# Optimization experiments

Measured on AMD Instinct MI355X. Metric: run time of the kernel, lower is better.

Reference implementation:

```python
import jax, jax.numpy as jnp
import numpy as np

B, D_IN, H1, H2, D_OUT = 1024, 2048, 4096, 4096, 1024

def setup_inputs() -> dict:
    key = jax.random.key(0)
    ks = jax.random.split(key, 8)
    scale = lambda fan_in: 1.0 / np.sqrt(fan_in)
    x  = jax.random.normal(ks[0], (B, D_IN), dtype=jnp.float32)
    W1 = jax.random.normal(ks[1], (H1, D_IN), dtype=jnp.float32) * scale(D_IN)
    b1 = jax.random.normal(ks[2], (H1,), dtype=jnp.float32) * scale(D_IN)
    W2 = jax.random.normal(ks[3], (H2, H1), dtype=jnp.float32) * scale(H1)
    b2 = jax.random.normal(ks[4], (H2,), dtype=jnp.float32) * scale(H1)
    W3 = jax.random.normal(ks[5], (D_OUT, H2), dtype=jnp.float32) * scale(H2)
    b3 = jax.random.normal(ks[6], (D_OUT,), dtype=jnp.float32) * scale(H2)
    b_taus = jnp.array([2.0, 1.0, 0.5], dtype=jnp.float32)
    return {"x": x, "W1": W1, "b1": b1, "W2": W2, "b2": b2, "W3": W3, "b3": b3, "b_taus": b_taus, "T": 10}

def reference(x, W1, b1, W2, b2, W3, b3, b_taus, T):
    # x: [B, D_IN] (already flat). betas are scalar sigmoid gates, constant over time.
    beta1, beta2, beta3 = jax.nn.sigmoid(b_taus)
    s1 = jnp.zeros((x.shape[0], W1.shape[0]), dtype=x.dtype)
    s2 = jnp.zeros((x.shape[0], W2.shape[0]), dtype=x.dtype)
    s3 = jnp.zeros((x.shape[0], W3.shape[0]), dtype=x.dtype)

    def step(carry, _):
        s1, s2, s3 = carry
        d1 = jax.nn.relu(x @ W1.T + b1)
        s1 = beta1 * s1 + (1 - beta1) * d1
        d2 = jax.nn.relu(s1 @ W2.T + b2)
        s2 = beta2 * s2 + (1 - beta2) * d2
        d3 = s2 @ W3.T + b3
        s3 = beta3 * s3 + (1 - beta3) * d3
        return (s1, s2, s3), None

    (s1, s2, s3), _ = jax.lax.scan(step, (s1, s2, s3), None, length=T)
    return s3
```

## Files before the change

kernel.cpp:

```cpp
#include <hip/hip_runtime.h>
#include <hip/hip_bf16.h>
#include <stdint.h>

#define AS_GLOBAL __attribute__((address_space(1)))
#define AS_LDS    __attribute__((address_space(3)))

typedef __attribute__((ext_vector_type(8))) short  bf16x8;
typedef __attribute__((ext_vector_type(4))) float  f32x4;
typedef __attribute__((ext_vector_type(4))) short  s16x4;
typedef __attribute__((ext_vector_type(8))) short  s16x8;

__device__ __forceinline__ void gload_lds16(const void* g, void* l) {
    __builtin_amdgcn_global_load_lds((AS_GLOBAL const void*)g, (AS_LDS void*)l, 16, 0, 0);
}

__device__ __forceinline__ void cast_pair(const float* __restrict__ s,
                                          __hip_bfloat16* __restrict__ d, long p) {
    f32x4 a = ((const f32x4*)s)[p * 2];
    f32x4 b = ((const f32x4*)s)[p * 2 + 1];
    union { s16x8 p8; __hip_bfloat16 h[8]; } u;
    u.h[0] = __float2bfloat16(a.x); u.h[1] = __float2bfloat16(a.y);
    u.h[2] = __float2bfloat16(a.z); u.h[3] = __float2bfloat16(a.w);
    u.h[4] = __float2bfloat16(b.x); u.h[5] = __float2bfloat16(b.y);
    u.h[6] = __float2bfloat16(b.z); u.h[7] = __float2bfloat16(b.w);
    ((s16x8*)d)[p] = u.p8;
}

__global__ void cast_a_k(const float* __restrict__ x,  __hip_bfloat16* __restrict__ xb,
                         const float* __restrict__ W1, __hip_bfloat16* __restrict__ W1b) {
    const long nx = 262144, ntot = 1310720, stride = 1280 * 256;
    long t = (long)blockIdx.x * 256 + threadIdx.x;
    for (long p = t; p < ntot; p += stride) {
        if (p < nx) cast_pair(x, xb, p);
        else        cast_pair(W1, W1b, p - nx);
    }
}

template <int FUSECAST>
__global__ __launch_bounds__(256, 3)
void gemm_btk(const __hip_bfloat16* __restrict__ A,
              const __hip_bfloat16* __restrict__ Bm,
              __hip_bfloat16* __restrict__ P,
              const int M, const int N, const int kchunk, const int S,
              const float* __restrict__ cs1, __hip_bfloat16* __restrict__ cd1, const long cn1,
              const float* __restrict__ cs2, __hip_bfloat16* __restrict__ cd2, const long cn2)
{
    __shared__ __hip_bfloat16 As[128 * 64];
    __shared__ __hip_bfloat16 Bs[128 * 64];

    const int tid = threadIdx.x;
    const int bn = blockIdx.x, bm = blockIdx.y, z = blockIdx.z;

    if (FUSECAST && z < FUSECAST) {
        const long nb     = (long)gridDim.x * gridDim.y;
        const long stride = FUSECAST * nb * 256;
        long t = ((long)z * nb + (long)bm * gridDim.x + bn) * 256 + tid;
        const long ntot = cn1 + cn2;
        for (long p = t; p < ntot; p += stride) {
            if (p < cn1) cast_pair(cs1, cd1, p);
            else         cast_pair(cs2, cd2, p - cn1);
        }
        return;
    }
    const int kz = z - FUSECAST;

    const int lane = tid & 63;
    const int wave = tid >> 6;
    const int wm   = wave >> 1, wn = wave & 1;
    const int lm   = lane & 15, lq = lane >> 4;

    const int K  = kchunk * S;
    const int k0 = kz * kchunk;

    const int rlo  = lane >> 3;
    const int gsw8 = (((lane & 7) ^ rlo) << 3);

    const __hip_bfloat16* Ag = A  + (size_t)(bm * 128) * K;
    const __hip_bfloat16* Bg = Bm + (size_t)(bn * 128) * K;

    f32x4 acc[4][4];
    #pragma unroll
    for (int i = 0; i < 4; ++i)
        #pragma unroll
        for (int j = 0; j < 4; ++j)
            acc[i][j] = (f32x4){0.f, 0.f, 0.f, 0.f};

    for (int kt = k0; kt < k0 + kchunk; kt += 64) {
        __syncthreads();
        #pragma unroll
        for (int c = 0; c < 4; ++c) {
            const int chunk = wave * 4 + c;
            const int row   = chunk * 8 + rlo;
            gload_lds16(Ag + (size_t)row * K + kt + gsw8, As + chunk * 512);
            gload_lds16(Bg + (size_t)row * K + kt + gsw8, Bs + chunk * 512);
        }
        __syncthreads();
        #pragma unroll
        for (int kk = 0; kk < 2; ++kk) {
            const int sl = (((kk * 4 + lq) ^ (lm & 7)) << 3);
            bf16x8 af[4], bf[4];
            #pragma unroll
            for (int i = 0; i < 4; ++i)
                af[i] = *(const bf16x8*)(As + (wm * 64 + i * 16 + lm) * 64 + sl);
            #pragma unroll
            for (int j = 0; j < 4; ++j)
                bf[j] = *(const bf16x8*)(Bs + (wn * 64 + j * 16 + lm) * 64 + sl);
            #pragma unroll
            for (int i = 0; i < 4; ++i)
                #pragma unroll
                for (int j = 0; j < 4; ++j)
                    acc[i][j] = __builtin_amdgcn_mfma_f32_16x16x32_bf16(af[i], bf[j], acc[i][j], 0, 0, 0);
        }
    }

    __hip_bfloat16* Pz = P + (size_t)kz * M * N;
    const int row0 = bm * 128 + wm * 64;
    const int colb = bn * 128 + wn * 64 + lm;
    #pragma unroll
    for (int j = 0; j < 4; ++j) {
        const int col = colb + j * 16;
        #pragma unroll
        for (int i = 0; i < 4; ++i)
            #pragma unroll
            for (int r = 0; r < 4; ++r) {
                const int row = row0 + i * 16 + lq * 4 + r;
                Pz[(size_t)row * N + col] = __float2bfloat16(acc[i][j][r]);
            }
    }
}

template <int TT>
__device__ __forceinline__ void tcollapse_coef(float be1, float be2, float be3,
                                               float* __restrict__ c, float* __restrict__ w) {
    float g[TT + 1];
    g[TT] = 1.f;
    float p3 = 1.f;
    #pragma unroll
    for (int u = TT - 1; u >= 1; --u) {
        p3 *= be3;
        g[u] = be2 * g[u + 1] + p3;
    }
    const float s = (1.f - be2) * (1.f - be3);
    float p1 = 1.f;
    #pragma unroll
    for (int u = 1; u <= TT; ++u) {
        p1 *= be1;
        c[u - 1] = 1.f - p1;
        w[u - 1] = s * g[u];
    }
}

template <int MODE>
__global__ void reduce_k(const __hip_bfloat16* __restrict__ P, const int S,
                         void* __restrict__ outv, const long MN, const int N,
                         const float* __restrict__ bias,
                         const float* __restrict__ b_taus,
                         const int* __restrict__ Tp)
{
    long i8 = (long)blockIdx.x * 256 + threadIdx.x;
    long i  = i8 * 8;
    float a[8] = {0.f, 0.f, 0.f, 0.f, 0.f, 0.f, 0.f, 0.f};
    for (int s = 0; s < S; ++s) {
        union { s16x8 p8; __hip_bfloat16 h[8]; } u;
        u.p8 = *(const s16x8*)(P + (size_t)s * MN + i);
        #pragma unroll
        for (int c = 0; c < 8; ++c) a[c] += __bfloat162float(u.h[c]);
    }
    const int col = (int)(i % N);
    float bb[8];
    #pragma unroll
    for (int c = 0; c < 8; ++c) bb[c] = bias[col + c];

    if constexpr (MODE == 0) {
        union { s16x8 p8; __hip_bfloat16 h[8]; } u;
        #pragma unroll
        for (int c = 0; c < 8; ++c)
            u.h[c] = __float2bfloat16(fmaxf(a[c] + bb[c], 0.f));
        ((s16x8*)outv)[i8] = u.p8;
    } else if constexpr (MODE == 1) {
        const int   T   = *Tp;
        const float be1 = 1.f / (1.f + expf(-b_taus[0]));
        const float be2 = 1.f / (1.f + expf(-b_taus[1]));
        const float be3 = 1.f / (1.f + expf(-b_taus[2]));
        union { s16x8 p8; __hip_bfloat16 h[8]; } u;
        if (T == 10) {
            float c10[10], w10[10];
            tcollapse_coef<10>(be1, be2, be3, c10, w10);
            #pragma unroll
            for (int c = 0; c < 8; ++c) {
                float za = 0.f;
                #pragma unroll
                for (int t = 0; t < 10; ++t)
                    za += w10[t] * fmaxf(fmaf(c10[t], a[c], bb[c]), 0.f);
                u.h[c] = __float2bfloat16(za);
            }
        } else {
            #pragma unroll
            for (int c = 0; c < 8; ++c) {
                float p1 = 1.f, s2 = 0.f, za = 0.f;
                for (int t = 0; t < T; ++t) {
                    p1 *= be1;
                    const float d2 = fmaxf(fmaf(1.f - p1, a[c], bb[c]), 0.f);
                    s2 = be2 * s2 + (1.f - be2) * d2;
                    za = be3 * za + (1.f - be3) * s2;
                }
                u.h[c] = __float2bfloat16(za);
            }
        }
        ((s16x8*)outv)[i8] = u.p8;
    } else {
        const int   T   = *Tp;
        const float be3 = 1.f / (1.f + expf(-b_taus[2]));
        float g = 0.f;
        for (int t = 0; t < T; ++t) g = be3 * g + (1.f - be3);
        f32x4 o0, o1;
        o0.x = a[0] + g * bb[0]; o0.y = a[1] + g * bb[1];
        o0.z = a[2] + g * bb[2]; o0.w = a[3] + g * bb[3];
        o1.x = a[4] + g * bb[4]; o1.y = a[5] + g * bb[5];
        o1.z = a[6] + g * bb[6]; o1.w = a[7] + g * bb[7];
        ((f32x4*)outv)[i8 * 2]     = o0;
        ((f32x4*)outv)[i8 * 2 + 1] = o1;
    }
}

extern "C" void kernel_launch(void* const* d_in, const int* in_sizes, int n_in,
                              void* d_out, int out_size, void* d_ws, size_t ws_size,
                              hipStream_t stream) {
    const float* x      = (const float*)d_in[0];
    const float* W1     = (const float*)d_in[1];
    const float* b1     = (const float*)d_in[2];
    const float* W2     = (const float*)d_in[3];
    const float* b2     = (const float*)d_in[4];
    const float* W3     = (const float*)d_in[5];
    const float* b3     = (const float*)d_in[6];
    const float* b_taus = (const float*)d_in[7];
    const int*   Tp     = (const int*)d_in[8];

    const int B = 1024, DIN = 2048, H1 = 4096, H2 = 4096, DOUT = 1024;
    const long MB = 1024 * 1024;

    char* ws = (char*)d_ws;
    __hip_bfloat16* xb  = (__hip_bfloat16*)(ws + 0);
    __hip_bfloat16* W1b = (__hip_bfloat16*)(ws + 4 * MB);
    __hip_bfloat16* W2b = (__hip_bfloat16*)(ws + 20 * MB);
    __hip_bfloat16* W3b = (__hip_bfloat16*)(ws + 52 * MB);
    __hip_bfloat16* D1b = (__hip_bfloat16*)(ws + 60 * MB);
    __hip_bfloat16* Sb  = (__hip_bfloat16*)(ws + 68 * MB);
    __hip_bfloat16* P1  = (__hip_bfloat16*)(ws + 76 * MB);
    __hip_bfloat16* P2  = (__hip_bfloat16*)(ws + 92 * MB);
    __hip_bfloat16* P3  = (__hip_bfloat16*)(ws + 124 * MB);

    cast_a_k<<<dim3(1280), dim3(256), 0, stream>>>(x, xb, W1, W1b);

    gemm_btk<1><<<dim3(H1 / 128, B / 128, 1 + 2), 256, 0, stream>>>(
        xb, W1b, P1, B, H1, DIN / 2, 2,
        W2, W2b, (long)H2 * H1 / 8, W3, W3b, (long)DOUT * H2 / 8);
    reduce_k<0><<<dim3(2048), 256, 0, stream>>>(P1, 2, (void*)D1b, (long)B * H1, H1, b1, nullptr, nullptr);

    gemm_btk<0><<<dim3(H2 / 128, B / 128, 4), 256, 0, stream>>>(
        D1b, W2b, P2, B, H2, H1 / 4, 4, nullptr, nullptr, 0, nullptr, nullptr, 0);
    reduce_k<1><<<dim3(2048), 256, 0, stream>>>(P2, 4, (void*)Sb, (long)B * H2, H2, b2, b_taus, Tp);

    gemm_btk<0><<<dim3(DOUT / 128, B / 128, 8), 256, 0, stream>>>(
        Sb, W3b, P3, B, DOUT, H2 / 8, 8, nullptr, nullptr, 0, nullptr, nullptr, 0);
    reduce_k<2><<<dim3(512), 256, 0, stream>>>(P3, 8, d_out, (long)B * DOUT, DOUT, b3, b_taus, Tp);
}
```

Before: 250.6 us.

## Double-buffer LDS in GEMM, remap blocks per XCD, halve layer-2 split-K

The GEMM kernel now keeps two LDS buffers for each operand. It issues the global-to-LDS loads for the next K tile before computing on the current one, which halves the barriers per tile and overlaps loads with MFMA work. Thread blocks are remapped so that consecutive hardware block IDs, which round-robin across the 8 XCDs, land on contiguous column tiles within each XCD, aiming for better L2 reuse. The second GEMM drops from 4 to 2 split-K slices, which shrinks the partial-sum buffer and the reduce work, and occupancy bounds are lowered from 3 to 2 blocks to fit the doubled LDS use.

After: 254.1 us. Within noise of the previous version (+1.4%).

```diff
diff --git a/kernel.cpp b/kernel.cpp
--- a/kernel.cpp
+++ b/kernel.cpp
@@ -37,7 +37,7 @@
 }
 
 template <int FUSECAST>
-__global__ __launch_bounds__(256, 3)
+__global__ __launch_bounds__(256, 2)
 void gemm_btk(const __hip_bfloat16* __restrict__ A,
               const __hip_bfloat16* __restrict__ Bm,
               __hip_bfloat16* __restrict__ P,
@@ -45,11 +45,12 @@
               const float* __restrict__ cs1, __hip_bfloat16* __restrict__ cd1, const long cn1,
               const float* __restrict__ cs2, __hip_bfloat16* __restrict__ cd2, const long cn2)
 {
-    __shared__ __hip_bfloat16 As[128 * 64];
-    __shared__ __hip_bfloat16 Bs[128 * 64];
+    __shared__ __hip_bfloat16 As[2][128 * 64];
+    __shared__ __hip_bfloat16 Bs[2][128 * 64];
 
     const int tid = threadIdx.x;
-    const int bn = blockIdx.x, bm = blockIdx.y, z = blockIdx.z;
+    int bn = blockIdx.x, bm = blockIdx.y;
+    const int z = blockIdx.z;
 
     if (FUSECAST && z < FUSECAST) {
         const long nb     = (long)gridDim.x * gridDim.y;
@@ -64,6 +65,16 @@
     }
     const int kz = z - FUSECAST;
 
+    const int Gx = gridDim.x;
+    if ((Gx & 7) == 0) {
+        const int bnx = Gx >> 3;
+        const int lid = bm * Gx + bn;
+        const int xcd = lid & 7;
+        const int ix  = lid >> 3;
+        bn = xcd * bnx + (ix % bnx);
+        bm = ix / bnx;
+    }
+
     const int lane = tid & 63;
     const int wave = tid >> 6;
     const int wm   = wave >> 1, wn = wave & 1;
@@ -78,38 +89,55 @@
     const __hip_bfloat16* Ag = A  + (size_t)(bm * 128) * K;
     const __hip_bfloat16* Bg = Bm + (size_t)(bn * 128) * K;
 
-    f32x4 acc[4][4];
-    #pragma unroll
-    for (int i = 0; i < 4; ++i)
-        #pragma unroll
-        for (int j = 0; j < 4; ++j)
-            acc[i][j] = (f32x4){0.f, 0.f, 0.f, 0.f};
-
-    for (int kt = k0; kt < k0 + kchunk; kt += 64) {
-        __syncthreads();
+    auto stage = [&](int d, int kt) {
         #pragma unroll
         for (int c = 0; c < 4; ++c) {
             const int chunk = wave * 4 + c;
             const int row   = chunk * 8 + rlo;
-            gload_lds16(Ag + (size_t)row * K + kt + gsw8, As + chunk * 512);
-            gload_lds16(Bg + (size_t)row * K + kt + gsw8, Bs + chunk * 512);
-        }
-        __syncthreads();
+            gload_lds16(Ag + (size_t)row * K + kt + gsw8, &As[d][chunk * 512]);
+            gload_lds16(Bg + (size_t)row * K + kt + gsw8, &Bs[d][chunk * 512]);
+        }
+    };
+
+    stage(0, k0);
+
+    f32x4 acc[4][4];
+    #pragma unroll
+    for (int i = 0; i < 4; ++i)
+        #pragma unroll
+        for (int j = 0; j < 4; ++j)
+            acc[i][j] = (f32x4){0.f, 0.f, 0.f, 0.f};
+
+    auto compute = [&](int d) {
         #pragma unroll
         for (int kk = 0; kk < 2; ++kk) {
             const int sl = (((kk * 4 + lq) ^ (lm & 7)) << 3);
-            bf16x8 af[4], bf[4];
+            bf16x8 af[4], bq[4];
             #pragma unroll
             for (int i = 0; i < 4; ++i)
-                af[i] = *(const bf16x8*)(As + (wm * 64 + i * 16 + lm) * 64 + sl);
+                af[i] = *(const bf16x8*)(&As[d][(wm * 64 + i * 16 + lm) * 64 + sl]);
             #pragma unroll
             for (int j = 0; j < 4; ++j)
-                bf[j] = *(const bf16x8*)(Bs + (wn * 64 + j * 16 + lm) * 64 + sl);
+                bq[j] = *(const bf16x8*)(&Bs[d][(wn * 64 + j * 16 + lm) * 64 + sl]);
             #pragma unroll
             for (int i = 0; i < 4; ++i)
                 #pragma unroll
                 for (int j = 0; j < 4; ++j)
-                    acc[i][j] = __builtin_amdgcn_mfma_f32_16x16x32_bf16(af[i], bf[j], acc[i][j], 0, 0, 0);
+                    acc[i][j] = __builtin_amdgcn_mfma_f32_16x16x32_bf16(af[i], bq[j], acc[i][j], 0, 0, 0);
+        }
+    };
+
+    const int kend = k0 + kchunk;
+    __syncthreads();
+
+    for (int kt = k0; kt < kend; kt += 128) {
+        if (kt + 64 < kend) stage(1, kt + 64);
+        compute(0);
+        __syncthreads();
+        if (kt + 64 < kend) {
+            if (kt + 128 < kend) stage(0, kt + 128);
+            compute(1);
+            __syncthreads();
         }
     }
 
@@ -257,9 +285,9 @@
         W2, W2b, (long)H2 * H1 / 8, W3, W3b, (long)DOUT * H2 / 8);
     reduce_k<0><<<dim3(2048), 256, 0, stream>>>(P1, 2, (void*)D1b, (long)B * H1, H1, b1, nullptr, nullptr);
 
-    gemm_btk<0><<<dim3(H2 / 128, B / 128, 4), 256, 0, stream>>>(
-        D1b, W2b, P2, B, H2, H1 / 4, 4, nullptr, nullptr, 0, nullptr, nullptr, 0);
-    reduce_k<1><<<dim3(2048), 256, 0, stream>>>(P2, 4, (void*)Sb, (long)B * H2, H2, b2, b_taus, Tp);
+    gemm_btk<0><<<dim3(H2 / 128, B / 128, 2), 256, 0, stream>>>(
+        D1b, W2b, P2, B, H2, H1 / 2, 2, nullptr, nullptr, 0, nullptr, nullptr, 0);
+    reduce_k<1><<<dim3(2048), 256, 0, stream>>>(P2, 2, (void*)Sb, (long)B * H2, H2, b2, b_taus, Tp);
 
     gemm_btk<0><<<dim3(DOUT / 128, B / 128, 8), 256, 0, stream>>>(
         Sb, W3b, P3, B, DOUT, H2 / 8, 8, nullptr, nullptr, 0, nullptr, nullptr, 0);
```

## Fuse fp32 weight-to-bf16 conversion into GEMM B-tile loads, add XCD block remap

Applied to the files above, without the earlier changes.

Drops the separate weight cast passes. Each GEMM now reads the fp32 weights directly, converts them to bf16 in registers and stores them into swizzled LDS, which removes the write and re-read of bf16 weight copies. Only x is still cast in its own small kernel. The change also remaps block indices so that neighbouring tiles land on the same XCD, and switches layer 1 to a 4-way K split with occupancy raised to 4. In exchange, the B operand now moves twice the bytes per tile through the synchronous register path instead of async global-to-LDS loads, and the W1 split gets more partial-sum traffic.

Result: slower. 325.3 us (+29.8%).

```diff
diff --git a/kernel.cpp b/kernel.cpp
--- a/kernel.cpp
+++ b/kernel.cpp
@@ -7,7 +7,6 @@
 
 typedef __attribute__((ext_vector_type(8))) short  bf16x8;
 typedef __attribute__((ext_vector_type(4))) float  f32x4;
-typedef __attribute__((ext_vector_type(4))) short  s16x4;
 typedef __attribute__((ext_vector_type(8))) short  s16x8;
 
 __device__ __forceinline__ void gload_lds16(const void* g, void* l) {
@@ -26,43 +25,33 @@
     ((s16x8*)d)[p] = u.p8;
 }
 
-__global__ void cast_a_k(const float* __restrict__ x,  __hip_bfloat16* __restrict__ xb,
-                         const float* __restrict__ W1, __hip_bfloat16* __restrict__ W1b) {
-    const long nx = 262144, ntot = 1310720, stride = 1280 * 256;
-    long t = (long)blockIdx.x * 256 + threadIdx.x;
-    for (long p = t; p < ntot; p += stride) {
-        if (p < nx) cast_pair(x, xb, p);
-        else        cast_pair(W1, W1b, p - nx);
-    }
-}
-
-template <int FUSECAST>
-__global__ __launch_bounds__(256, 3)
-void gemm_btk(const __hip_bfloat16* __restrict__ A,
-              const __hip_bfloat16* __restrict__ Bm,
-              __hip_bfloat16* __restrict__ P,
-              const int M, const int N, const int kchunk, const int S,
-              const float* __restrict__ cs1, __hip_bfloat16* __restrict__ cd1, const long cn1,
-              const float* __restrict__ cs2, __hip_bfloat16* __restrict__ cd2, const long cn2)
+__global__ void cast_x_k(const float* __restrict__ x, __hip_bfloat16* __restrict__ xb) {
+    long p = (long)blockIdx.x * 256 + threadIdx.x;
+    cast_pair(x, xb, p);
+}
+
+__global__ __launch_bounds__(256, 4)
+void gemm_bf(const __hip_bfloat16* __restrict__ A,
+             const float* __restrict__ Bf,
+             __hip_bfloat16* __restrict__ P,
+             const int M, const int N, const int kchunk, const int S)
 {
     __shared__ __hip_bfloat16 As[128 * 64];
     __shared__ __hip_bfloat16 Bs[128 * 64];
 
     const int tid = threadIdx.x;
-    const int bn = blockIdx.x, bm = blockIdx.y, z = blockIdx.z;
-
-    if (FUSECAST && z < FUSECAST) {
-        const long nb     = (long)gridDim.x * gridDim.y;
-        const long stride = FUSECAST * nb * 256;
-        long t = ((long)z * nb + (long)bm * gridDim.x + bn) * 256 + tid;
-        const long ntot = cn1 + cn2;
-        for (long p = t; p < ntot; p += stride) {
-            if (p < cn1) cast_pair(cs1, cd1, p);
-            else         cast_pair(cs2, cd2, p - cn1);
-        }
-        return;
-    }
-    const int kz = z - FUSECAST;
+    int bn = blockIdx.x, bm = blockIdx.y;
+    const int kz = blockIdx.z;
+
+    const int Gx = gridDim.x;
+    if ((Gx & 7) == 0) {
+        const int bnx = Gx >> 3;
+        const int lid = bm * Gx + bn;
+        const int xcd = lid & 7;
+        const int ix  = lid >> 3;
+        bn = xcd * bnx + (ix % bnx);
+        bm = ix / bnx;
+    }
 
     const int lane = tid & 63;
     const int wave = tid >> 6;
@@ -73,10 +62,11 @@
     const int k0 = kz * kchunk;
 
     const int rlo  = lane >> 3;
-    const int gsw8 = (((lane & 7) ^ rlo) << 3);
+    const int g    = lane & 7;
+    const int gsw8 = ((g ^ rlo) << 3);
 
     const __hip_bfloat16* Ag = A  + (size_t)(bm * 128) * K;
-    const __hip_bfloat16* Bg = Bm + (size_t)(bn * 128) * K;
+    const float*          Bg = Bf + (size_t)(bn * 128) * K;
 
     f32x4 acc[4][4];
     #pragma unroll
@@ -87,29 +77,46 @@
 
     for (int kt = k0; kt < k0 + kchunk; kt += 64) {
         __syncthreads();
+        f32x4 bl[4][2];
+        #pragma unroll
+        for (int c = 0; c < 4; ++c) {
+            const int row = (wave * 4 + c) * 8 + rlo;
+            const float* p = Bg + (size_t)row * K + kt + g * 8;
+            bl[c][0] = *(const f32x4*)p;
+            bl[c][1] = *(const f32x4*)(p + 4);
+        }
         #pragma unroll
         for (int c = 0; c < 4; ++c) {
             const int chunk = wave * 4 + c;
             const int row   = chunk * 8 + rlo;
             gload_lds16(Ag + (size_t)row * K + kt + gsw8, As + chunk * 512);
-            gload_lds16(Bg + (size_t)row * K + kt + gsw8, Bs + chunk * 512);
+        }
+        #pragma unroll
+        for (int c = 0; c < 4; ++c) {
+            const int chunk = wave * 4 + c;
+            union { s16x8 p8; __hip_bfloat16 h[8]; } u;
+            u.h[0] = __float2bfloat16(bl[c][0].x); u.h[1] = __float2bfloat16(bl[c][0].y);
+            u.h[2] = __float2bfloat16(bl[c][0].z); u.h[3] = __float2bfloat16(bl[c][0].w);
+            u.h[4] = __float2bfloat16(bl[c][1].x); u.h[5] = __float2bfloat16(bl[c][1].y);
+            u.h[6] = __float2bfloat16(bl[c][1].z); u.h[7] = __float2bfloat16(bl[c][1].w);
+            *(s16x8*)(Bs + chunk * 512 + rlo * 64 + gsw8) = u.p8;
         }
         __syncthreads();
         #pragma unroll
         for (int kk = 0; kk < 2; ++kk) {
             const int sl = (((kk * 4 + lq) ^ (lm & 7)) << 3);
-            bf16x8 af[4], bf[4];
+            bf16x8 af[4], bq[4];
             #pragma unroll
             for (int i = 0; i < 4; ++i)
                 af[i] = *(const bf16x8*)(As + (wm * 64 + i * 16 + lm) * 64 + sl);
             #pragma unroll
             for (int j = 0; j < 4; ++j)
-                bf[j] = *(const bf16x8*)(Bs + (wn * 64 + j * 16 + lm) * 64 + sl);
+                bq[j] = *(const bf16x8*)(Bs + (wn * 64 + j * 16 + lm) * 64 + sl);
             #pragma unroll
             for (int i = 0; i < 4; ++i)
                 #pragma unroll
                 for (int j = 0; j < 4; ++j)
-                    acc[i][j] = __builtin_amdgcn_mfma_f32_16x16x32_bf16(af[i], bf[j], acc[i][j], 0, 0, 0);
+                    acc[i][j] = __builtin_amdgcn_mfma_f32_16x16x32_bf16(af[i], bq[j], acc[i][j], 0, 0, 0);
         }
     }
 
@@ -241,27 +248,23 @@
 
     char* ws = (char*)d_ws;
     __hip_bfloat16* xb  = (__hip_bfloat16*)(ws + 0);
-    __hip_bfloat16* W1b = (__hip_bfloat16*)(ws + 4 * MB);
-    __hip_bfloat16* W2b = (__hip_bfloat16*)(ws + 20 * MB);
-    __hip_bfloat16* W3b = (__hip_bfloat16*)(ws + 52 * MB);
-    __hip_bfloat16* D1b = (__hip_bfloat16*)(ws + 60 * MB);
-    __hip_bfloat16* Sb  = (__hip_bfloat16*)(ws + 68 * MB);
-    __hip_bfloat16* P1  = (__hip_bfloat16*)(ws + 76 * MB);
-    __hip_bfloat16* P2  = (__hip_bfloat16*)(ws + 92 * MB);
-    __hip_bfloat16* P3  = (__hip_bfloat16*)(ws + 124 * MB);
-
-    cast_a_k<<<dim3(1280), dim3(256), 0, stream>>>(x, xb, W1, W1b);
-
-    gemm_btk<1><<<dim3(H1 / 128, B / 128, 1 + 2), 256, 0, stream>>>(
-        xb, W1b, P1, B, H1, DIN / 2, 2,
-        W2, W2b, (long)H2 * H1 / 8, W3, W3b, (long)DOUT * H2 / 8);
-    reduce_k<0><<<dim3(2048), 256, 0, stream>>>(P1, 2, (void*)D1b, (long)B * H1, H1, b1, nullptr, nullptr);
-
-    gemm_btk<0><<<dim3(H2 / 128, B / 128, 4), 256, 0, stream>>>(
-        D1b, W2b, P2, B, H2, H1 / 4, 4, nullptr, nullptr, 0, nullptr, nullptr, 0);
+    __hip_bfloat16* D1b = (__hip_bfloat16*)(ws + 4 * MB);
+    __hip_bfloat16* Sb  = (__hip_bfloat16*)(ws + 12 * MB);
+    __hip_bfloat16* P1  = (__hip_bfloat16*)(ws + 20 * MB);
+    __hip_bfloat16* P2  = (__hip_bfloat16*)(ws + 52 * MB);
+    __hip_bfloat16* P3  = (__hip_bfloat16*)(ws + 84 * MB);
+
+    cast_x_k<<<dim3(1024), dim3(256), 0, stream>>>(x, xb);
+
+    gemm_bf<<<dim3(H1 / 128, B / 128, 4), 256, 0, stream>>>(
+        xb, W1, P1, B, H1, DIN / 4, 4);
+    reduce_k<0><<<dim3(2048), 256, 0, stream>>>(P1, 4, (void*)D1b, (long)B * H1, H1, b1, nullptr, nullptr);
+
+    gemm_bf<<<dim3(H2 / 128, B / 128, 4), 256, 0, stream>>>(
+        D1b, W2, P2, B, H2, H1 / 4, 4);
     reduce_k<1><<<dim3(2048), 256, 0, stream>>>(P2, 4, (void*)Sb, (long)B * H2, H2, b2, b_taus, Tp);
 
-    gemm_btk<0><<<dim3(DOUT / 128, B / 128, 8), 256, 0, stream>>>(
-        Sb, W3b, P3, B, DOUT, H2 / 8, 8, nullptr, nullptr, 0, nullptr, nullptr, 0);
+    gemm_bf<<<dim3(DOUT / 128, B / 128, 8), 256, 0, stream>>>(
+        Sb, W3, P3, B, DOUT, H2 / 8, 8);
     reduce_k<2><<<dim3(512), 256, 0, stream>>>(P3, 8, d_out, (long)B * DOUT, DOUT, b3, b_taus, Tp);
 }
```
